# Performance work log

Hardware: AMD Instinct MI355X
Metric: run time of the kernel (lower is better)

Reference implementation:

```python
import jax, jax.numpy as jnp
import numpy as np

N = 20000          # num_nodes
E = 320000         # num_edges
D = 128            # node_dim
HID = 128          # hidden_dim
OUT = 128          # output_dim
H = 4              # num_heads
C1 = HID // H      # 32, per-head dim layer 0 (concat)
C2 = OUT           # 128, per-head dim last layer (mean over heads)
EPS = 1e-5


def _glorot(k, shape):
    fan_in, fan_out = shape
    s = (6.0 / (fan_in + fan_out)) ** 0.5
    return jax.random.uniform(k, shape, minval=-s, maxval=s, dtype=jnp.float32)


def setup_inputs() -> dict:
    key = jax.random.key(0)
    ks = jax.random.split(key, 24)
    inp = {
        "x": jax.random.normal(ks[0], (N, D), dtype=jnp.float32),
        "edge_index": jax.random.randint(ks[1], (2, E), 0, N, dtype=jnp.int64),
        "W_in": _glorot(ks[2], (D, HID)), "b_in": jnp.zeros((HID,), jnp.float32),
        # layer 0: in=HID, heads*out = H*C1 = HID
        "Wq1": _glorot(ks[3], (HID, H * C1)), "bq1": jnp.zeros((H * C1,), jnp.float32),
        "Wk1": _glorot(ks[4], (HID, H * C1)), "bk1": jnp.zeros((H * C1,), jnp.float32),
        "Wv1": _glorot(ks[5], (HID, H * C1)), "bv1": jnp.zeros((H * C1,), jnp.float32),
        "att1": _glorot(ks[6], (H, 2 * C1)).reshape(1, H, 2 * C1),
        "g1": jnp.ones((HID,), jnp.float32), "beta1": jnp.zeros((HID,), jnp.float32),
        # layer 1 (last): in=HID, heads*out = H*C2
        "Wq2": _glorot(ks[7], (HID, H * C2)), "bq2": jnp.zeros((H * C2,), jnp.float32),
        "Wk2": _glorot(ks[8], (HID, H * C2)), "bk2": jnp.zeros((H * C2,), jnp.float32),
        "Wv2": _glorot(ks[9], (HID, H * C2)), "bv2": jnp.zeros((H * C2,), jnp.float32),
        "att2": _glorot(ks[10], (H, 2 * C2)).reshape(1, H, 2 * C2),
        "g2": jnp.ones((OUT,), jnp.float32), "beta2": jnp.zeros((OUT,), jnp.float32),
        "W_out": _glorot(ks[11], (OUT, OUT)), "b_out": jnp.zeros((OUT,), jnp.float32),
    }
    return inp


def _gat(h, src, dst, Wq, bq, Wk, bk, Wv, bv, att, heads, c):
    # q,k,v: [N, H, C]
    q = (h @ Wq + bq).reshape(-1, heads, c)
    k = (h @ Wk + bk).reshape(-1, heads, c)
    v = (h @ Wv + bv).reshape(-1, heads, c)
    qi = q[dst]            # [E, H, C] target-node query
    kj = k[src]            # [E, H, C] source-node key
    vj = v[src]            # [E, H, C]
    alpha = (jnp.concatenate([qi, kj], axis=-1) * att).sum(-1)  # [E, H]
    # segment softmax over incoming edges of each target node
    m = jax.ops.segment_max(alpha, dst, num_segments=N)         # [N, H]
    ex = jnp.exp(alpha - m[dst])
    s = jax.ops.segment_sum(ex, dst, num_segments=N)            # [N, H]
    a = ex / jnp.maximum(s, 1e-16)[dst]                         # [E, H]
    msg = vj * a[..., None]
    return jax.ops.segment_sum(msg, dst, num_segments=N)        # [N, H, C]


def _ln(x, g, b):
    mu = x.mean(-1, keepdims=True)
    var = ((x - mu) ** 2).mean(-1, keepdims=True)
    return (x - mu) * jax.lax.rsqrt(var + EPS) * g + b


def reference(x, edge_index, W_in, b_in, Wq1, bq1, Wk1, bk1, Wv1, bv1, att1, g1, beta1,
              Wq2, bq2, Wk2, bk2, Wv2, bv2, att2, g2, beta2, W_out, b_out):
    src = edge_index[0]  # source node j
    dst = edge_index[1]  # target node i
    h = jax.nn.relu(x @ W_in + b_in)                               # [N, HID]
    # layer 0: concat heads -> [N, H*C1] = [N, HID], residual, LN, ReLU
    o1 = _gat(h, src, dst, Wq1, bq1, Wk1, bk1, Wv1, bv1, att1, H, C1).reshape(-1, H * C1)
    h = jax.nn.relu(_ln(o1 + h, g1, beta1))
    # layer 1: mean over heads -> [N, OUT], residual (HID==OUT), LN
    o2 = _gat(h, src, dst, Wq2, bq2, Wk2, bk2, Wv2, bv2, att2, H, C2).mean(axis=1)
    h = _ln(o2 + h, g2, beta2)
    z = h @ W_out + b_out                                          # [N, OUT]
    return z
```

## Files before the change

kernel.cpp:

```cpp
#include <hip/hip_runtime.h>
#include <hip/hip_bf16.h>
#include <math.h>

#define N_NODES 20000
#define N_EDGES 320000
#define DIM     128
#define HIDDEN  128
#define NH      4
#define C1      32
#define C2      128
#define VC1     132
#define VC2     516
#define LN_EPS  1e-5f

__device__ __forceinline__ float wave_sum(float v){
#pragma unroll
  for (int o = 32; o; o >>= 1) v += __shfl_xor(v, o, 64);
  return v;
}
__device__ __forceinline__ float wave_max(float v){
#pragma unroll
  for (int o = 32; o; o >>= 1) v = fmaxf(v, __shfl_xor(v, o, 64));
  return v;
}

__global__ __launch_bounds__(1024) void detect_kernel(const int* __restrict__ ei32,
                                                      int* __restrict__ flag){
  __shared__ int any;
  if (threadIdx.x == 0) any = 0;
  __syncthreads();
  if (ei32[2 * threadIdx.x + 1] != 0) atomicOr(&any, 1);
  __syncthreads();
  if (threadIdx.x == 0) *flag = (any == 0) ? 1 : 0;
}

__global__ void hist_kernel(const int* __restrict__ ei, const int* __restrict__ flag,
                            int* __restrict__ counts){
  const bool wide = (*flag != 0);
  for (int e = blockIdx.x * blockDim.x + threadIdx.x; e < N_EDGES;
       e += gridDim.x * blockDim.x){
    int d = wide ? ei[2 * (N_EDGES + e)] : ei[N_EDGES + e];
    atomicAdd(&counts[d], 1);
  }
}

__global__ __launch_bounds__(1024) void scan_kernel(const int* __restrict__ counts,
    int* __restrict__ row_ptr, int* __restrict__ fill_ptr){
  const int PER = 20;
  int t = threadIdx.x;
  int base = t * PER;
  int local[PER];
  int s = 0;
#pragma unroll
  for (int i = 0; i < PER; i++){
    int idx = base + i;
    int c = (idx < N_NODES) ? counts[idx] : 0;
    s += c; local[i] = s;
  }
  __shared__ int bs[1024];
  bs[t] = s; __syncthreads();
  for (int off = 1; off < 1024; off <<= 1){
    int v = (t >= off) ? bs[t - off] : 0;
    __syncthreads();
    bs[t] += v;
    __syncthreads();
  }
  int excl = bs[t] - s;
  int prev = 0;
#pragma unroll
  for (int i = 0; i < PER; i++){
    int idx = base + i;
    if (idx < N_NODES){
      row_ptr[idx + 1] = excl + local[i];
      fill_ptr[idx]    = excl + prev;
    }
    prev = local[i];
  }
  if (t == 0) row_ptr[0] = 0;
}

__global__ void scatter_kernel(const int* __restrict__ ei, const int* __restrict__ flag,
                               int* __restrict__ fill_ptr, int* __restrict__ col_idx){
  const bool wide = (*flag != 0);
  for (int e = blockIdx.x * blockDim.x + threadIdx.x; e < N_EDGES;
       e += gridDim.x * blockDim.x){
    int d = wide ? ei[2 * (N_EDGES + e)] : ei[N_EDGES + e];
    int s = wide ? ei[2 * e]             : ei[e];
    int pos = atomicAdd(&fill_ptr[d], 1);
    col_idx[pos] = s;
  }
}

__global__ void prep_ak_weights(const float* __restrict__ Wk1, const float* __restrict__ att1,
                                const float* __restrict__ Wk2, const float* __restrict__ att2,
                                float* __restrict__ Wka1, float* __restrict__ Wka2){
  int tid = blockIdx.x * blockDim.x + threadIdx.x;
  int stride = gridDim.x * blockDim.x;
  for (int idx = tid; idx < 128 * NH; idx += stride){
    int k = idx >> 2, h = idx & 3;
    float s = 0.f;
    for (int c = 0; c < C1; c++)
      s += Wk1[k * 128 + h * C1 + c] * att1[h * 2 * C1 + C1 + c];
    Wka1[idx] = s;
  }
  for (int idx = tid; idx < 128 * NH; idx += stride){
    int k = idx >> 2, h = idx & 3;
    float s = 0.f;
    for (int c = 0; c < C2; c++)
      s += Wk2[k * 512 + h * C2 + c] * att2[h * 2 * C2 + C2 + c];
    Wka2[idx] = s;
  }
}

__global__ __launch_bounds__(256) void akgemv(const float* __restrict__ hin,
    const float* __restrict__ Wka, float* __restrict__ vcat, int V, int VC){
  int wid = threadIdx.x >> 6, lane = threadIdx.x & 63;
  int n = blockIdx.x * 4 + wid;
  if (n >= N_NODES) return;
  float2 hv = *(const float2*)&hin[(size_t)n * 128 + (lane << 1)];
  float4 wa = *(const float4*)&Wka[lane << 3];
  float4 wb = *(const float4*)&Wka[(lane << 3) + 4];
  float p0 = hv.x * wa.x + hv.y * wb.x;
  float p1 = hv.x * wa.y + hv.y * wb.y;
  float p2 = hv.x * wa.z + hv.y * wb.z;
  float p3 = hv.x * wa.w + hv.y * wb.w;
  p0 = wave_sum(p0); p1 = wave_sum(p1); p2 = wave_sum(p2); p3 = wave_sum(p3);
  if (lane == 0)
    *(float4*)&vcat[(size_t)n * VC + V] = make_float4(p0, p1, p2, p3);
}

template <int ACT>
__global__ __launch_bounds__(256) void gemm_tile(const float* __restrict__ X,
    const float* __restrict__ W, const float* __restrict__ bias,
    float* __restrict__ Y, int M, int ldY){
  __shared__ float XsT[64][68];
  __shared__ float Ws[64][64];
  const int t = threadIdx.x;
  const int row0 = blockIdx.x * 64;
  const int j0 = blockIdx.y * 64;
  const int ra = (t >> 4) << 2;
  const int cb = (t & 15) << 2;
  float acc[4][4] = {{0.f}};
#pragma unroll
  for (int k0 = 0; k0 < 128; k0 += 64){
    if (k0) __syncthreads();
#pragma unroll
    for (int i = 0; i < 4; i++){
      int idx4 = t + i * 256;
      int r = idx4 >> 4;
      int c4 = (idx4 & 15) << 2;
      int grow = row0 + r; if (grow >= N_NODES) grow = N_NODES - 1;
      float4 v = *(const float4*)&X[(size_t)grow * 128 + k0 + c4];
      XsT[c4][r] = v.x; XsT[c4 + 1][r] = v.y;
      XsT[c4 + 2][r] = v.z; XsT[c4 + 3][r] = v.w;
    }
#pragma unroll
    for (int i = 0; i < 4; i++){
      int idx4 = t + i * 256;
      int k = idx4 >> 4;
      int c4 = (idx4 & 15) << 2;
      *(float4*)&Ws[k][c4] = *(const float4*)&W[(size_t)(k0 + k) * M + j0 + c4];
    }
    __syncthreads();
#pragma unroll 8
    for (int k = 0; k < 64; k++){
      float4 xv = *(const float4*)&XsT[k][ra];
      float4 wv = *(const float4*)&Ws[k][cb];
      acc[0][0] = fmaf(xv.x, wv.x, acc[0][0]); acc[0][1] = fmaf(xv.x, wv.y, acc[0][1]);
      acc[0][2] = fmaf(xv.x, wv.z, acc[0][2]); acc[0][3] = fmaf(xv.x, wv.w, acc[0][3]);
      acc[1][0] = fmaf(xv.y, wv.x, acc[1][0]); acc[1][1] = fmaf(xv.y, wv.y, acc[1][1]);
      acc[1][2] = fmaf(xv.y, wv.z, acc[1][2]); acc[1][3] = fmaf(xv.y, wv.w, acc[1][3]);
      acc[2][0] = fmaf(xv.z, wv.x, acc[2][0]); acc[2][1] = fmaf(xv.z, wv.y, acc[2][1]);
      acc[2][2] = fmaf(xv.z, wv.z, acc[2][2]); acc[2][3] = fmaf(xv.z, wv.w, acc[2][3]);
      acc[3][0] = fmaf(xv.w, wv.x, acc[3][0]); acc[3][1] = fmaf(xv.w, wv.y, acc[3][1]);
      acc[3][2] = fmaf(xv.w, wv.z, acc[3][2]); acc[3][3] = fmaf(xv.w, wv.w, acc[3][3]);
    }
  }
  const float4 b4 = *(const float4*)&bias[j0 + cb];
#pragma unroll
  for (int i = 0; i < 4; i++){
    int orow = row0 + ra + i;
    if (orow >= N_NODES) break;
    float4 o;
    o.x = acc[i][0] + b4.x; o.y = acc[i][1] + b4.y;
    o.z = acc[i][2] + b4.z; o.w = acc[i][3] + b4.w;
    if (ACT == 1){
      o.x = fmaxf(o.x, 0.f); o.y = fmaxf(o.y, 0.f);
      o.z = fmaxf(o.z, 0.f); o.w = fmaxf(o.w, 0.f);
    }
    *(float4*)&Y[(size_t)orow * ldY + j0 + cb] = o;
  }
}

__global__ __launch_bounds__(256) void gat0(const float* __restrict__ vcat,
    const int* __restrict__ row_ptr, const int* __restrict__ col_idx,
    const float* __restrict__ hres, const float* __restrict__ g,
    const float* __restrict__ beta, float* __restrict__ out){
  __shared__ float exs[4][256];
  int wid = threadIdx.x >> 6;
  int lane = threadIdx.x & 63;
  int n = blockIdx.x * 4 + wid;
  if (n >= N_NODES) return;
  int start = row_ptr[n], end = row_ptr[n + 1];
  float m0 = -1e30f, m1 = -1e30f, m2 = -1e30f, m3 = -1e30f;
  for (int e = start + lane; e < end; e += 64){
    int s = col_idx[e];
    const float4 ak = *(const float4*)&vcat[(size_t)s * VC1 + 128];
    m0 = fmaxf(m0, ak.x); m1 = fmaxf(m1, ak.y);
    m2 = fmaxf(m2, ak.z); m3 = fmaxf(m3, ak.w);
  }
  m0 = wave_max(m0); m1 = wave_max(m1); m2 = wave_max(m2); m3 = wave_max(m3);
  int l5 = lane >> 5;
  int c4 = (lane & 31) << 2;
  int h  = (lane & 31) >> 3;
  float a0 = 0.f, a1 = 0.f, a2 = 0.f, a3 = 0.f;
  float s0 = 0.f, s1 = 0.f, s2 = 0.f, s3 = 0.f;
  for (int base = start; base < end; base += 64){
    int e = base + lane;
    float4 ex = make_float4(0.f, 0.f, 0.f, 0.f);
    int srcj = 0;
    if (e < end){
      srcj = col_idx[e];
      const float4 ak = *(const float4*)&vcat[(size_t)srcj * VC1 + 128];
      ex.x = __expf(ak.x - m0); ex.y = __expf(ak.y - m1);
      ex.z = __expf(ak.z - m2); ex.w = __expf(ak.w - m3);
      s0 += ex.x; s1 += ex.y; s2 += ex.z; s3 += ex.w;
    }
    *(float4*)&exs[wid][lane << 2] = ex;
    __builtin_amdgcn_wave_barrier();
    int cnt = end - base; if (cnt > 64) cnt = 64;
    int half = (cnt + 1) >> 1;
    for (int j = 0; j < half; ++j){
      int jj = 2 * j + l5;
      int jjc = (jj < cnt) ? jj : 0;
      int sj = __shfl(srcj, jjc, 64);
      if (jj < cnt){
        float eh = exs[wid][(jj << 2) + h];
        const float4 v = *(const float4*)&vcat[(size_t)sj * VC1 + c4];
        a0 = fmaf(eh, v.x, a0); a1 = fmaf(eh, v.y, a1);
        a2 = fmaf(eh, v.z, a2); a3 = fmaf(eh, v.w, a3);
      }
    }
    __builtin_amdgcn_wave_barrier();
  }
  a0 += __shfl_xor(a0, 32, 64); a1 += __shfl_xor(a1, 32, 64);
  a2 += __shfl_xor(a2, 32, 64); a3 += __shfl_xor(a3, 32, 64);
  s0 = wave_sum(s0); s1 = wave_sum(s1); s2 = wave_sum(s2); s3 = wave_sum(s3);
  float sh = (h == 0) ? s0 : (h == 1) ? s1 : (h == 2) ? s2 : s3;
  sh = fmaxf(sh, 1e-16f);
  float inv = 1.f / sh;
  const float4 r = *(const float4*)&hres[(size_t)n * HIDDEN + c4];
  float v0 = a0 * inv + r.x, v1 = a1 * inv + r.y;
  float v2 = a2 * inv + r.z, v3 = a3 * inv + r.w;
  float mean = wave_sum(v0 + v1 + v2 + v3) * (1.f / 256.f);
  float d0 = v0 - mean, d1 = v1 - mean, d2 = v2 - mean, d3 = v3 - mean;
  float var = wave_sum(d0*d0 + d1*d1 + d2*d2 + d3*d3) * (1.f / 256.f);
  float rs = rsqrtf(var + LN_EPS);
  const float4 g4 = *(const float4*)&g[c4];
  const float4 b4 = *(const float4*)&beta[c4];
  if (l5 == 0){
    float4 o;
    o.x = fmaxf(d0 * rs * g4.x + b4.x, 0.f);
    o.y = fmaxf(d1 * rs * g4.y + b4.y, 0.f);
    o.z = fmaxf(d2 * rs * g4.z + b4.z, 0.f);
    o.w = fmaxf(d3 * rs * g4.w + b4.w, 0.f);
    *(float4*)&out[(size_t)n * HIDDEN + c4] = o;
  }
}

__global__ __launch_bounds__(256) void gat1(const float* __restrict__ vcat,
    const int* __restrict__ row_ptr, const int* __restrict__ col_idx,
    const float* __restrict__ hres, const float* __restrict__ g,
    const float* __restrict__ beta, float* __restrict__ out){
  __shared__ float exs[4][256];
  int wid = threadIdx.x >> 6;
  int lane = threadIdx.x & 63;
  int n = blockIdx.x * 4 + wid;
  if (n >= N_NODES) return;
  int start = row_ptr[n], end = row_ptr[n + 1];
  float m0 = -1e30f, m1 = -1e30f, m2 = -1e30f, m3 = -1e30f;
  for (int e = start + lane; e < end; e += 64){
    int s = col_idx[e];
    const float4 ak = *(const float4*)&vcat[(size_t)s * VC2 + 512];
    m0 = fmaxf(m0, ak.x); m1 = fmaxf(m1, ak.y);
    m2 = fmaxf(m2, ak.z); m3 = fmaxf(m3, ak.w);
  }
  m0 = wave_max(m0); m1 = wave_max(m1); m2 = wave_max(m2); m3 = wave_max(m3);
  int l5 = lane >> 5;
  int c4 = (lane & 31) << 2;
  int hA = l5 << 1;
  float a0 = 0, a1 = 0, a2 = 0, a3 = 0;
  float b0 = 0, b1 = 0, b2 = 0, b3 = 0;
  float s0 = 0.f, s1 = 0.f, s2 = 0.f, s3 = 0.f;
  for (int base = start; base < end; base += 64){
    int e = base + lane;
    float4 ex = make_float4(0.f, 0.f, 0.f, 0.f);
    int srcj = 0;
    if (e < end){
      srcj = col_idx[e];
      const float4 ak = *(const float4*)&vcat[(size_t)srcj * VC2 + 512];
      ex.x = __expf(ak.x - m0); ex.y = __expf(ak.y - m1);
      ex.z = __expf(ak.z - m2); ex.w = __expf(ak.w - m3);
      s0 += ex.x; s1 += ex.y; s2 += ex.z; s3 += ex.w;
    }
    *(float4*)&exs[wid][lane << 2] = ex;
    __builtin_amdgcn_wave_barrier();
    int cnt = end - base; if (cnt > 64) cnt = 64;
    for (int j = 0; j < cnt; ++j){
      int sj = __shfl(srcj, j, 64);
      const float2 eh = *(const float2*)&exs[wid][(j << 2) + (l5 << 1)];
      const float* vr = &vcat[(size_t)sj * VC2 + (hA << 7) + c4];
      const float4 va = *(const float4*)(vr);
      const float4 vb = *(const float4*)(vr + 128);
      a0 = fmaf(eh.x, va.x, a0); a1 = fmaf(eh.x, va.y, a1);
      a2 = fmaf(eh.x, va.z, a2); a3 = fmaf(eh.x, va.w, a3);
      b0 = fmaf(eh.y, vb.x, b0); b1 = fmaf(eh.y, vb.y, b1);
      b2 = fmaf(eh.y, vb.z, b2); b3 = fmaf(eh.y, vb.w, b3);
    }
    __builtin_amdgcn_wave_barrier();
  }
  s0 = wave_sum(s0); s1 = wave_sum(s1); s2 = wave_sum(s2); s3 = wave_sum(s3);
  float sA = (l5 == 0) ? s0 : s2;
  float sB = (l5 == 0) ? s1 : s3;
  sA = 1.f / fmaxf(sA, 1e-16f);
  sB = 1.f / fmaxf(sB, 1e-16f);
  float t0 = a0 * sA + b0 * sB;
  float t1 = a1 * sA + b1 * sB;
  float t2 = a2 * sA + b2 * sB;
  float t3 = a3 * sA + b3 * sB;
  t0 += __shfl_xor(t0, 32, 64); t1 += __shfl_xor(t1, 32, 64);
  t2 += __shfl_xor(t2, 32, 64); t3 += __shfl_xor(t3, 32, 64);
  const float4 r = *(const float4*)&hres[(size_t)n * HIDDEN + c4];
  float v0 = 0.25f * t0 + r.x, v1 = 0.25f * t1 + r.y;
  float v2 = 0.25f * t2 + r.z, v3 = 0.25f * t3 + r.w;
  float mean = wave_sum(v0 + v1 + v2 + v3) * (1.f / 256.f);
  float d0 = v0 - mean, d1 = v1 - mean, d2 = v2 - mean, d3 = v3 - mean;
  float var = wave_sum(d0*d0 + d1*d1 + d2*d2 + d3*d3) * (1.f / 256.f);
  float rs = rsqrtf(var + LN_EPS);
  const float4 g4 = *(const float4*)&g[c4];
  const float4 b4 = *(const float4*)&beta[c4];
  if (l5 == 0){
    float4 o;
    o.x = d0 * rs * g4.x + b4.x;
    o.y = d1 * rs * g4.y + b4.y;
    o.z = d2 * rs * g4.z + b4.z;
    o.w = d3 * rs * g4.w + b4.w;
    *(float4*)&out[(size_t)n * HIDDEN + c4] = o;
  }
}

extern "C" void kernel_launch(void* const* d_in, const int* in_sizes, int n_in,
                              void* d_out, int out_size, void* d_ws, size_t ws_size,
                              hipStream_t stream) {
  const float* x     = (const float*)d_in[0];
  const int*   ei    = (const int*)  d_in[1];
  const float* W_in  = (const float*)d_in[2];
  const float* b_in  = (const float*)d_in[3];
  const float* Wk1   = (const float*)d_in[6];
  const float* Wv1   = (const float*)d_in[8];
  const float* bv1   = (const float*)d_in[9];
  const float* att1  = (const float*)d_in[10];
  const float* g1    = (const float*)d_in[11];
  const float* beta1 = (const float*)d_in[12];
  const float* Wk2   = (const float*)d_in[15];
  const float* Wv2   = (const float*)d_in[17];
  const float* bv2   = (const float*)d_in[18];
  const float* att2  = (const float*)d_in[19];
  const float* g2    = (const float*)d_in[20];
  const float* beta2 = (const float*)d_in[21];
  const float* W_out = (const float*)d_in[22];
  const float* b_out = (const float*)d_in[23];
  float* zout = (float*)d_out;

  char* base = (char*)d_ws;
  size_t off = 0;
  auto take = [&](size_t bytes) -> void* {
    void* p = base + off;
    off += (bytes + 255) & ~(size_t)255;
    return p;
  };
  float* h1      = (float*)take((size_t)N_NODES * 128 * 4);
  float* h2      = (float*)take((size_t)N_NODES * 128 * 4);
  float* vcat2   = (float*)take((size_t)N_NODES * VC2 * 4);
  float* vcat1   = vcat2;
  float* Wka1    = (float*)take(128 * NH * 4);
  float* Wka2    = (float*)take(128 * NH * 4);
  int*   counts  = (int*)take((size_t)N_NODES * 4);
  int*   row_ptr = (int*)take((size_t)(N_NODES + 1) * 4);
  int*   fillp   = (int*)take((size_t)N_NODES * 4);
  int*   col_idx = (int*)take((size_t)N_EDGES * 4);
  int*   eflag   = (int*)take(256);
  float* h3      = h1;

  const int RT = (N_NODES + 63) / 64;

  hipMemsetAsync(counts, 0, (size_t)N_NODES * 4, stream);
  detect_kernel<<<1, 1024, 0, stream>>>(ei, eflag);
  hist_kernel<<<512, 256, 0, stream>>>(ei, eflag, counts);
  scan_kernel<<<1, 1024, 0, stream>>>(counts, row_ptr, fillp);
  scatter_kernel<<<512, 256, 0, stream>>>(ei, eflag, fillp, col_idx);

  prep_ak_weights<<<2, 256, 0, stream>>>(Wk1, att1, Wk2, att2, Wka1, Wka2);

  gemm_tile<1><<<dim3(RT, 2), 256, 0, stream>>>(x, W_in, b_in, h1, 128, 128);
  gemm_tile<0><<<dim3(RT, 2), 256, 0, stream>>>(h1, Wv1, bv1, vcat1, 128, VC1);
  akgemv<<<(N_NODES + 3) / 4, 256, 0, stream>>>(h1, Wka1, vcat1, 128, VC1);
  gat0<<<N_NODES / 4, 256, 0, stream>>>(vcat1, row_ptr, col_idx, h1, g1, beta1, h2);
  gemm_tile<0><<<dim3(RT, 8), 256, 0, stream>>>(h2, Wv2, bv2, vcat2, 512, VC2);
  akgemv<<<(N_NODES + 3) / 4, 256, 0, stream>>>(h2, Wka2, vcat2, 512, VC2);
  gat1<<<N_NODES / 4, 256, 0, stream>>>(vcat2, row_ptr, col_idx, h2, g2, beta2, h3);
  gemm_tile<0><<<dim3(RT, 2), 256, 0, stream>>>(h3, W_out, b_out, zout, 128, 128);
}
```

Measured before the change: 412.1 us.

## Aggregate layer-2 inputs before value projection to shrink gathered rows

Layer 2 no longer projects every node to a 512-wide value tensor before the edge gather. It gathers the 128-wide h2 rows with per-head softmax weights into a 512-wide per-node buffer u, then applies a single K=512 GEMM against a reordered Wv2 with the head-mean folded into weights and bias. This cuts per-edge gather traffic from 512 floats to 128 and replaces an N×128×512 GEMM with an N×512×128 one. It adds a separate layernorm-residual kernel, a weight-reorder prep kernel and an extra intermediate write and read of u.

```diff
diff --git a/kernel.cpp b/kernel.cpp
--- a/kernel.cpp
+++ b/kernel.cpp
@@ -10,7 +10,6 @@
 #define C1      32
 #define C2      128
 #define VC1     132
-#define VC2     516
 #define LN_EPS  1e-5f
 
 __device__ __forceinline__ float wave_sum(float v){
@@ -112,8 +111,31 @@
   }
 }
 
+__global__ void prep_w2r(const float* __restrict__ Wv2, const float* __restrict__ bv2,
+                         float* __restrict__ W2r, float* __restrict__ mb){
+  int tid = blockIdx.x * blockDim.x + threadIdx.x;
+  if (tid < 16384){
+    int hk = tid >> 5;
+    int c4 = (tid & 31) << 2;
+    int h = hk >> 7, k = hk & 127;
+    *(float4*)&W2r[(size_t)hk * 128 + c4] =
+        *(const float4*)&Wv2[(size_t)k * 512 + h * 128 + c4];
+  }
+  if (tid < 32){
+    int c4 = tid << 2;
+    float4 b0 = *(const float4*)&bv2[c4];
+    float4 b1 = *(const float4*)&bv2[128 + c4];
+    float4 b2 = *(const float4*)&bv2[256 + c4];
+    float4 b3 = *(const float4*)&bv2[384 + c4];
+    *(float4*)&mb[c4] = make_float4(0.25f * (b0.x + b1.x + b2.x + b3.x),
+                                    0.25f * (b0.y + b1.y + b2.y + b3.y),
+                                    0.25f * (b0.z + b1.z + b2.z + b3.z),
+                                    0.25f * (b0.w + b1.w + b2.w + b3.w));
+  }
+}
+
 __global__ __launch_bounds__(256) void akgemv(const float* __restrict__ hin,
-    const float* __restrict__ Wka, float* __restrict__ vcat, int V, int VC){
+    const float* __restrict__ Wka, float* __restrict__ dst, int V, int VC){
   int wid = threadIdx.x >> 6, lane = threadIdx.x & 63;
   int n = blockIdx.x * 4 + wid;
   if (n >= N_NODES) return;
@@ -126,10 +148,10 @@
   float p3 = hv.x * wa.w + hv.y * wb.w;
   p0 = wave_sum(p0); p1 = wave_sum(p1); p2 = wave_sum(p2); p3 = wave_sum(p3);
   if (lane == 0)
-    *(float4*)&vcat[(size_t)n * VC + V] = make_float4(p0, p1, p2, p3);
-}
-
-template <int ACT>
+    *(float4*)&dst[(size_t)n * VC + V] = make_float4(p0, p1, p2, p3);
+}
+
+template <int ACT, int K>
 __global__ __launch_bounds__(256) void gemm_tile(const float* __restrict__ X,
     const float* __restrict__ W, const float* __restrict__ bias,
     float* __restrict__ Y, int M, int ldY){
@@ -141,8 +163,7 @@
   const int ra = (t >> 4) << 2;
   const int cb = (t & 15) << 2;
   float acc[4][4] = {{0.f}};
-#pragma unroll
-  for (int k0 = 0; k0 < 128; k0 += 64){
+  for (int k0 = 0; k0 < K; k0 += 64){
     if (k0) __syncthreads();
 #pragma unroll
     for (int i = 0; i < 4; i++){
@@ -150,7 +171,7 @@
       int r = idx4 >> 4;
       int c4 = (idx4 & 15) << 2;
       int grow = row0 + r; if (grow >= N_NODES) grow = N_NODES - 1;
-      float4 v = *(const float4*)&X[(size_t)grow * 128 + k0 + c4];
+      float4 v = *(const float4*)&X[(size_t)grow * K + k0 + c4];
       XsT[c4][r] = v.x; XsT[c4 + 1][r] = v.y;
       XsT[c4 + 2][r] = v.z; XsT[c4 + 3][r] = v.w;
     }
@@ -268,10 +289,10 @@
   }
 }
 
-__global__ __launch_bounds__(256) void gat1(const float* __restrict__ vcat,
+__global__ __launch_bounds__(256) void gat1_agg(const float* __restrict__ h2,
+    const float* __restrict__ ak2,
     const int* __restrict__ row_ptr, const int* __restrict__ col_idx,
-    const float* __restrict__ hres, const float* __restrict__ g,
-    const float* __restrict__ beta, float* __restrict__ out){
+    float* __restrict__ u){
   __shared__ float exs[4][256];
   int wid = threadIdx.x >> 6;
   int lane = threadIdx.x & 63;
@@ -280,17 +301,14 @@
   int start = row_ptr[n], end = row_ptr[n + 1];
   float m0 = -1e30f, m1 = -1e30f, m2 = -1e30f, m3 = -1e30f;
   for (int e = start + lane; e < end; e += 64){
-    int s = col_idx[e];
-    const float4 ak = *(const float4*)&vcat[(size_t)s * VC2 + 512];
-    m0 = fmaxf(m0, ak.x); m1 = fmaxf(m1, ak.y);
-    m2 = fmaxf(m2, ak.z); m3 = fmaxf(m3, ak.w);
+    const float4 a = *(const float4*)&ak2[(size_t)col_idx[e] * 4];
+    m0 = fmaxf(m0, a.x); m1 = fmaxf(m1, a.y);
+    m2 = fmaxf(m2, a.z); m3 = fmaxf(m3, a.w);
   }
   m0 = wave_max(m0); m1 = wave_max(m1); m2 = wave_max(m2); m3 = wave_max(m3);
   int l5 = lane >> 5;
   int c4 = (lane & 31) << 2;
-  int hA = l5 << 1;
-  float a0 = 0, a1 = 0, a2 = 0, a3 = 0;
-  float b0 = 0, b1 = 0, b2 = 0, b3 = 0;
+  float acc[4][4] = {{0.f}};
   float s0 = 0.f, s1 = 0.f, s2 = 0.f, s3 = 0.f;
   for (int base = start; base < end; base += 64){
     int e = base + lane;
@@ -298,55 +316,71 @@
     int srcj = 0;
     if (e < end){
       srcj = col_idx[e];
-      const float4 ak = *(const float4*)&vcat[(size_t)srcj * VC2 + 512];
-      ex.x = __expf(ak.x - m0); ex.y = __expf(ak.y - m1);
-      ex.z = __expf(ak.z - m2); ex.w = __expf(ak.w - m3);
+      const float4 a = *(const float4*)&ak2[(size_t)srcj * 4];
+      ex.x = __expf(a.x - m0); ex.y = __expf(a.y - m1);
+      ex.z = __expf(a.z - m2); ex.w = __expf(a.w - m3);
       s0 += ex.x; s1 += ex.y; s2 += ex.z; s3 += ex.w;
     }
     *(float4*)&exs[wid][lane << 2] = ex;
     __builtin_amdgcn_wave_barrier();
     int cnt = end - base; if (cnt > 64) cnt = 64;
-    for (int j = 0; j < cnt; ++j){
-      int sj = __shfl(srcj, j, 64);
-      const float2 eh = *(const float2*)&exs[wid][(j << 2) + (l5 << 1)];
-      const float* vr = &vcat[(size_t)sj * VC2 + (hA << 7) + c4];
-      const float4 va = *(const float4*)(vr);
-      const float4 vb = *(const float4*)(vr + 128);
-      a0 = fmaf(eh.x, va.x, a0); a1 = fmaf(eh.x, va.y, a1);
-      a2 = fmaf(eh.x, va.z, a2); a3 = fmaf(eh.x, va.w, a3);
-      b0 = fmaf(eh.y, vb.x, b0); b1 = fmaf(eh.y, vb.y, b1);
-      b2 = fmaf(eh.y, vb.z, b2); b3 = fmaf(eh.y, vb.w, b3);
+    int half = (cnt + 1) >> 1;
+    for (int j = 0; j < half; ++j){
+      int jj = 2 * j + l5;
+      int jjc = (jj < cnt) ? jj : 0;
+      int sj = __shfl(srcj, jjc, 64);
+      if (jj < cnt){
+        const float4 eh = *(const float4*)&exs[wid][jj << 2];
+        const float4 v = *(const float4*)&h2[(size_t)sj * 128 + c4];
+        acc[0][0] = fmaf(eh.x, v.x, acc[0][0]); acc[0][1] = fmaf(eh.x, v.y, acc[0][1]);
+        acc[0][2] = fmaf(eh.x, v.z, acc[0][2]); acc[0][3] = fmaf(eh.x, v.w, acc[0][3]);
+        acc[1][0] = fmaf(eh.y, v.x, acc[1][0]); acc[1][1] = fmaf(eh.y, v.y, acc[1][1]);
+        acc[1][2] = fmaf(eh.y, v.z, acc[1][2]); acc[1][3] = fmaf(eh.y, v.w, acc[1][3]);
+        acc[2][0] = fmaf(eh.z, v.x, acc[2][0]); acc[2][1] = fmaf(eh.z, v.y, acc[2][1]);
+        acc[2][2] = fmaf(eh.z, v.z, acc[2][2]); acc[2][3] = fmaf(eh.z, v.w, acc[2][3]);
+        acc[3][0] = fmaf(eh.w, v.x, acc[3][0]); acc[3][1] = fmaf(eh.w, v.y, acc[3][1]);
+        acc[3][2] = fmaf(eh.w, v.z, acc[3][2]); acc[3][3] = fmaf(eh.w, v.w, acc[3][3]);
+      }
     }
     __builtin_amdgcn_wave_barrier();
   }
+#pragma unroll
+  for (int h = 0; h < 4; h++)
+#pragma unroll
+    for (int c = 0; c < 4; c++)
+      acc[h][c] += __shfl_xor(acc[h][c], 32, 64);
   s0 = wave_sum(s0); s1 = wave_sum(s1); s2 = wave_sum(s2); s3 = wave_sum(s3);
-  float sA = (l5 == 0) ? s0 : s2;
-  float sB = (l5 == 0) ? s1 : s3;
-  sA = 1.f / fmaxf(sA, 1e-16f);
-  sB = 1.f / fmaxf(sB, 1e-16f);
-  float t0 = a0 * sA + b0 * sB;
-  float t1 = a1 * sA + b1 * sB;
-  float t2 = a2 * sA + b2 * sB;
-  float t3 = a3 * sA + b3 * sB;
-  t0 += __shfl_xor(t0, 32, 64); t1 += __shfl_xor(t1, 32, 64);
-  t2 += __shfl_xor(t2, 32, 64); t3 += __shfl_xor(t3, 32, 64);
-  const float4 r = *(const float4*)&hres[(size_t)n * HIDDEN + c4];
-  float v0 = 0.25f * t0 + r.x, v1 = 0.25f * t1 + r.y;
-  float v2 = 0.25f * t2 + r.z, v3 = 0.25f * t3 + r.w;
-  float mean = wave_sum(v0 + v1 + v2 + v3) * (1.f / 256.f);
-  float d0 = v0 - mean, d1 = v1 - mean, d2 = v2 - mean, d3 = v3 - mean;
-  float var = wave_sum(d0*d0 + d1*d1 + d2*d2 + d3*d3) * (1.f / 256.f);
+  float w0 = 0.25f / fmaxf(s0, 1e-16f);
+  float w1 = 0.25f / fmaxf(s1, 1e-16f);
+  float w2 = 0.25f / fmaxf(s2, 1e-16f);
+  float w3 = 0.25f / fmaxf(s3, 1e-16f);
+  if (l5 == 0){
+    float* ur = &u[(size_t)n * 512 + c4];
+    *(float4*)(ur)       = make_float4(acc[0][0]*w0, acc[0][1]*w0, acc[0][2]*w0, acc[0][3]*w0);
+    *(float4*)(ur + 128) = make_float4(acc[1][0]*w1, acc[1][1]*w1, acc[1][2]*w1, acc[1][3]*w1);
+    *(float4*)(ur + 256) = make_float4(acc[2][0]*w2, acc[2][1]*w2, acc[2][2]*w2, acc[2][3]*w2);
+    *(float4*)(ur + 384) = make_float4(acc[3][0]*w3, acc[3][1]*w3, acc[3][2]*w3, acc[3][3]*w3);
+  }
+}
+
+__global__ __launch_bounds__(256) void ln_res(const float* __restrict__ o2,
+    const float* hres, const float* __restrict__ g,
+    const float* __restrict__ beta, float* out){
+  int wid = threadIdx.x >> 6, lane = threadIdx.x & 63;
+  int n = blockIdx.x * 4 + wid;
+  if (n >= N_NODES) return;
+  int c2 = lane << 1;
+  float2 a = *(const float2*)&o2[(size_t)n * 128 + c2];
+  float2 r = *(const float2*)&hres[(size_t)n * 128 + c2];
+  float vx = a.x + r.x, vy = a.y + r.y;
+  float mean = wave_sum(vx + vy) * (1.f / 128.f);
+  float dx = vx - mean, dy = vy - mean;
+  float var = wave_sum(dx * dx + dy * dy) * (1.f / 128.f);
   float rs = rsqrtf(var + LN_EPS);
-  const float4 g4 = *(const float4*)&g[c4];
-  const float4 b4 = *(const float4*)&beta[c4];
-  if (l5 == 0){
-    float4 o;
-    o.x = d0 * rs * g4.x + b4.x;
-    o.y = d1 * rs * g4.y + b4.y;
-    o.z = d2 * rs * g4.z + b4.z;
-    o.w = d3 * rs * g4.w + b4.w;
-    *(float4*)&out[(size_t)n * HIDDEN + c4] = o;
-  }
+  float2 gg = *(const float2*)&g[c2];
+  float2 bb = *(const float2*)&beta[c2];
+  *(float2*)&out[(size_t)n * 128 + c2] =
+      make_float2(dx * rs * gg.x + bb.x, dy * rs * gg.y + bb.y);
 }
 
 extern "C" void kernel_launch(void* const* d_in, const int* in_sizes, int n_in,
@@ -381,16 +415,20 @@
   };
   float* h1      = (float*)take((size_t)N_NODES * 128 * 4);
   float* h2      = (float*)take((size_t)N_NODES * 128 * 4);
-  float* vcat2   = (float*)take((size_t)N_NODES * VC2 * 4);
-  float* vcat1   = vcat2;
+  float* u       = (float*)take((size_t)N_NODES * 512 * 4);
+  float* vcat1   = u;
+  float* ak2     = (float*)take((size_t)N_NODES * 4 * 4);
   float* Wka1    = (float*)take(128 * NH * 4);
   float* Wka2    = (float*)take(128 * NH * 4);
+  float* W2r     = (float*)take(512 * 128 * 4);
+  float* mb      = (float*)take(128 * 4);
   int*   counts  = (int*)take((size_t)N_NODES * 4);
   int*   row_ptr = (int*)take((size_t)(N_NODES + 1) * 4);
   int*   fillp   = (int*)take((size_t)N_NODES * 4);
   int*   col_idx = (int*)take((size_t)N_EDGES * 4);
   int*   eflag   = (int*)take(256);
-  float* h3      = h1;
+  float* o2      = h1;
+  float* h3      = h2;
 
   const int RT = (N_NODES + 63) / 64;
 
@@ -401,13 +439,15 @@
   scatter_kernel<<<512, 256, 0, stream>>>(ei, eflag, fillp, col_idx);
 
   prep_ak_weights<<<2, 256, 0, stream>>>(Wk1, att1, Wk2, att2, Wka1, Wka2);
-
-  gemm_tile<1><<<dim3(RT, 2), 256, 0, stream>>>(x, W_in, b_in, h1, 128, 128);
-  gemm_tile<0><<<dim3(RT, 2), 256, 0, stream>>>(h1, Wv1, bv1, vcat1, 128, VC1);
+  prep_w2r<<<64, 256, 0, stream>>>(Wv2, bv2, W2r, mb);
+
+  gemm_tile<1, 128><<<dim3(RT, 2), 256, 0, stream>>>(x, W_in, b_in, h1, 128, 128);
+  gemm_tile<0, 128><<<dim3(RT, 2), 256, 0, stream>>>(h1, Wv1, bv1, vcat1, 128, VC1);
   akgemv<<<(N_NODES + 3) / 4, 256, 0, stream>>>(h1, Wka1, vcat1, 128, VC1);
   gat0<<<N_NODES / 4, 256, 0, stream>>>(vcat1, row_ptr, col_idx, h1, g1, beta1, h2);
-  gemm_tile<0><<<dim3(RT, 8), 256, 0, stream>>>(h2, Wv2, bv2, vcat2, 512, VC2);
-  akgemv<<<(N_NODES + 3) / 4, 256, 0, stream>>>(h2, Wka2, vcat2, 512, VC2);
-  gat1<<<N_NODES / 4, 256, 0, stream>>>(vcat2, row_ptr, col_idx, h2, g2, beta2, h3);
-  gemm_tile<0><<<dim3(RT, 2), 256, 0, stream>>>(h3, W_out, b_out, zout, 128, 128);
-}
+  akgemv<<<(N_NODES + 3) / 4, 256, 0, stream>>>(h2, Wka2, ak2, 0, 4);
+  gat1_agg<<<N_NODES / 4, 256, 0, stream>>>(h2, ak2, row_ptr, col_idx, u);
+  gemm_tile<0, 512><<<dim3(RT, 2), 256, 0, stream>>>(u, W2r, mb, o2, 128, 128);
+  ln_res<<<N_NODES / 4, 256, 0, stream>>>(o2, h2, g2, beta2, h3);
+  gemm_tile<0, 128><<<dim3(RT, 2), 256, 0, stream>>>(h3, W_out, b_out, zout, 128, 128);
+}
```

Measured after the change: 363.0 us. 11.9% less time.
